# Kernel optimization log

Measured on AMD Instinct MI355X. Metric: run time of the kernel, lower is better.

The kernel has to match this reference:

```python
import jax, jax.numpy as jnp
import numpy as np

INV_DELTA = 15.0  # inv_delta init kwarg


def setup_inputs() -> dict:
    key = jax.random.key(0)
    k1, k2 = jax.random.split(key)
    features = jax.random.normal(k1, (64, 1024, 14, 14), dtype=jnp.float32)
    # torch init: randn(num_words, num_channels).clamp(min=0)
    embedding = jnp.clip(jax.random.normal(k2, (8192, 1024), dtype=jnp.float32), 0.0, None)
    min_distance_mean = jnp.ones((1,), dtype=jnp.float32) * 0.5  # buffer init
    return {"features": features, "embedding": embedding,
            "min_distance_mean": min_distance_mean}


def reference(features, embedding, min_distance_mean):
    # BoWExtractor.forward in eval mode (no dictionary queue update / EMA).
    f = features[:, :, 1:-1, 1:-1]                      # [B,C,12,12] crop border
    emb_sq = jnp.sum(embedding * embedding, axis=1)     # [K]  ||w_k||^2
    cross = jnp.einsum('bchw,kc->bkhw', f, embedding)   # 1x1 conv == GEMM
    # squared L2 distance to every codeword: [B,K,12,12]
    dist = jnp.sum(f * f, axis=1, keepdims=True) - 2.0 * cross \
           + emb_sq[None, :, None, None]
    inv_delta_adaptive = INV_DELTA / min_distance_mean[0]
    codes = jax.nn.softmax(-inv_delta_adaptive * dist, axis=1)  # soft assignment over K
    bow = jnp.max(codes, axis=(2, 3))                   # global max-pool -> [B,K]
    bow = bow / jnp.sum(jnp.abs(bow), axis=1, keepdims=True)  # L1 normalize
    return bow, codes
```

## Files before the change

### kernel.cpp

```cpp
#include <hip/hip_runtime.h>
#include <math.h>

#define BB   64
#define CC   1024
#define HWC  144
#define KK   8192
#define MM   9216
#define NBN  128

typedef __attribute__((ext_vector_type(8)))  short          bf16x8;
typedef __attribute__((ext_vector_type(8)))  unsigned short u16x8;
typedef __attribute__((ext_vector_type(4)))  unsigned short u16x4;
typedef __attribute__((ext_vector_type(4)))  float          f32x4;
typedef __attribute__((ext_vector_type(16))) float          f32x16;

#define FA_BYTES  ((size_t)MM * CC * 2 * 2)
#define FB_BYTES  ((size_t)KK * CC * 2 * 2)
#define OFF_FA    0
#define OFF_FB    (OFF_FA + FA_BYTES)
#define OFF_ESQ   (OFF_FB + FB_BYTES)
#define OFF_PM    (OFF_ESQ + (size_t)KK * 4)
#define OFF_PS    (OFF_PM + (size_t)NBN * MM * 4)
#define OFF_FACT  (OFF_PS + (size_t)NBN * MM * 4)
#define OFF_E     (OFF_FACT + (size_t)NBN * MM * 4)
#define E_BYTES   ((size_t)BB * KK * HWC * 2)
#define WS_NEED_B16 (OFF_E + E_BYTES)

__device__ inline unsigned short f2bf(float x) {
    union { float f; unsigned u; } v; v.f = x;
    unsigned r = v.u + 0x7fffu + ((v.u >> 16) & 1u);
    return (unsigned short)(r >> 16);
}
__device__ inline float bf2f(unsigned short h) {
    union { unsigned u; float f; } v; v.u = (unsigned)h << 16;
    return v.f;
}

__global__ __launch_bounds__(256)
void prep_A(const float* __restrict__ feat, u16x8* __restrict__ fA) {
    __shared__ float tile[64][145];
    int cb = blockIdx.x;
    int b  = blockIdx.y;
    for (int idx = threadIdx.x; idx < 64 * 144; idx += 256) {
        int r = idx / 144, hw = idx - r * 144;
        int h = hw / 12, w = hw - h * 12;
        tile[r][hw] = feat[(size_t)((b * 1024 + cb * 64 + r) * 196)
                           + (h + 1) * 14 + (w + 1)];
    }
    __syncthreads();
    for (int idx = threadIdx.x; idx < 8 * 144; idx += 256) {
        int g = idx / 144, hw = idx - g * 144;
        int p = b * 144 + hw;
        int bm = p >> 8, row = p & 255;
        int c = cb * 64 + g * 8;
        int kt = c >> 4, oct = (c >> 3) & 1;
        u16x8 hi, lo;
#pragma unroll
        for (int e = 0; e < 8; ++e) {
            float x = tile[g * 8 + e][hw];
            unsigned short h16 = f2bf(x);
            hi[e] = (short)h16;
            lo[e] = (short)f2bf(x - bf2f(h16));
        }
        size_t base = ((size_t)bm * 64 + kt) * 1024 + oct * 256 + row;
        fA[base] = hi;
        fA[base + 512] = lo;
    }
}

__global__ __launch_bounds__(256)
void prep_B(const float* __restrict__ emb, u16x8* __restrict__ fB) {
    __shared__ float tile[128][65];
    int cb = blockIdx.x;
    int nb = blockIdx.y;
#pragma unroll
    for (int i = 0; i < 8; ++i) {
        int idx = threadIdx.x + i * 256;
        int nl = idx >> 4, c4 = idx & 15;
        const float4 v = *reinterpret_cast<const float4*>(
            emb + (size_t)(nb * 128 + nl) * 1024 + cb * 64 + c4 * 4);
        tile[nl][c4 * 4 + 0] = v.x;
        tile[nl][c4 * 4 + 1] = v.y;
        tile[nl][c4 * 4 + 2] = v.z;
        tile[nl][c4 * 4 + 3] = v.w;
    }
    __syncthreads();
#pragma unroll
    for (int i = 0; i < 4; ++i) {
        int idx = threadIdx.x + i * 256;
        int kc = idx >> 7, rl = idx & 127;
        int c = cb * 64 + kc * 8;
        int kt = c >> 4, oct = (c >> 3) & 1;
        u16x8 hi, lo;
#pragma unroll
        for (int e = 0; e < 8; ++e) {
            float x = tile[rl][kc * 8 + e];
            unsigned short h16 = f2bf(x);
            hi[e] = (short)h16;
            lo[e] = (short)f2bf(x - bf2f(h16));
        }
        size_t base = ((size_t)nb * 64 + kt) * 512 + oct * 128 + rl;
        fB[base] = hi;
        fB[base + 256] = lo;
    }
}

__global__ void rowsumsq(const float* __restrict__ src, float* __restrict__ dst) {
    int row = blockIdx.x * 4 + (threadIdx.x >> 6);
    int l = threadIdx.x & 63;
    const float4* p = reinterpret_cast<const float4*>(src + (size_t)row * 1024);
    float s = 0.f;
#pragma unroll
    for (int it = 0; it < 4; ++it) {
        float4 v = p[l + it * 64];
        s += v.x * v.x + v.y * v.y + v.z * v.z + v.w * v.w;
    }
#pragma unroll
    for (int off = 32; off; off >>= 1) s += __shfl_down(s, off);
    if (l == 0) dst[row] = s;
}

__global__ __launch_bounds__(256, 2)
void gemm_mfma(const char* __restrict__ fA, const char* __restrict__ fB,
               const float* __restrict__ esq, const float* __restrict__ mdm,
               float* __restrict__ codes, float* __restrict__ pm,
               float* __restrict__ ps, unsigned short* __restrict__ Ebf,
               int ebf16) {
    __shared__ __align__(16) char smem[73728];

    int flat = blockIdx.x;
    int swz = (flat & 7) * 288 + (flat >> 3);
    int bm = swz >> 6, bn = swz & 63;

    int tid = threadIdx.x;
    int l = tid & 63, l31 = l & 31, lc2 = l >> 5;
    int wv = tid >> 6, wr = wv >> 1, wc = wv & 1;

    const char* gA = fA + (size_t)bm * 1048576;
    const char* gB = fB + (size_t)bn * 524288;

    f32x16 acc[4][2];
#pragma unroll
    for (int i = 0; i < 4; ++i)
#pragma unroll
        for (int j = 0; j < 2; ++j)
#pragma unroll
            for (int r = 0; r < 16; ++r) acc[i][j][r] = 0.f;

    auto stage = [&](int buf, int kt) {
        char* db = smem + buf * 24576;
        const char* ga = gA + (size_t)kt * 16384;
        const char* gb = gB + (size_t)kt * 8192;
#pragma unroll
        for (int i = 0; i < 4; ++i) {
            int off = i * 4096 + tid * 16;
            __builtin_amdgcn_global_load_lds(
                (const __attribute__((address_space(1))) void*)(ga + off),
                (__attribute__((address_space(3))) void*)(db + off), 16, 0, 0);
        }
#pragma unroll
        for (int i = 0; i < 2; ++i) {
            int off = i * 4096 + tid * 16;
            __builtin_amdgcn_global_load_lds(
                (const __attribute__((address_space(1))) void*)(gb + off),
                (__attribute__((address_space(3))) void*)(db + 16384 + off), 16, 0, 0);
        }
    };

    stage(0, 0);
    stage(1, 1);
    stage(2, 2);

    int cur = 0;
    for (int kt = 0; kt < 64; ++kt) {
        asm volatile("s_waitcnt vmcnt(12)" ::: "memory");
        __builtin_amdgcn_s_barrier();
        __builtin_amdgcn_sched_barrier(0);

        const char* bufc = smem + cur * 24576;
        bf16x8 ah[4], al[4], bh[2], bl[2];
#pragma unroll
        for (int f = 0; f < 4; ++f) {
            int ao = (lc2 * 256 + wr * 128 + f * 32 + l31) * 16;
            ah[f] = *(const bf16x8*)(bufc + ao);
            al[f] = *(const bf16x8*)(bufc + 8192 + ao);
        }
#pragma unroll
        for (int f = 0; f < 2; ++f) {
            int bo = 16384 + (lc2 * 128 + wc * 64 + f * 32 + l31) * 16;
            bh[f] = *(const bf16x8*)(bufc + bo);
            bl[f] = *(const bf16x8*)(bufc + 4096 + bo);
        }
        __builtin_amdgcn_s_setprio(1);
#pragma unroll
        for (int fi = 0; fi < 4; ++fi)
#pragma unroll
            for (int fj = 0; fj < 2; ++fj) {
                f32x16& A = acc[fi][fj];
                A = __builtin_amdgcn_mfma_f32_32x32x16_bf16(ah[fi], bh[fj], A, 0, 0, 0);
                A = __builtin_amdgcn_mfma_f32_32x32x16_bf16(ah[fi], bl[fj], A, 0, 0, 0);
                A = __builtin_amdgcn_mfma_f32_32x32x16_bf16(al[fi], bh[fj], A, 0, 0, 0);
            }
        __builtin_amdgcn_s_setprio(0);
        __builtin_amdgcn_s_barrier();
        int kn = (kt + 3 > 63) ? 63 : kt + 3;
        stage(cur, kn);
        cur = (cur == 2) ? 0 : cur + 1;
    }
    asm volatile("s_waitcnt vmcnt(0)" ::: "memory");

    float invl2 = (15.0f / mdm[0]) * 1.44269504089f;
    float s2 = 2.0f * invl2;
    float e2[2];
#pragma unroll
    for (int fj = 0; fj < 2; ++fj)
        e2[fj] = invl2 * esq[bn * 128 + wc * 64 + fj * 32 + l31];

    int bnp = bn * 2 + wc;

#pragma unroll
    for (int fi = 0; fi < 4; ++fi) {
        float mx[16], ss[16];
#pragma unroll
        for (int fj = 0; fj < 2; ++fj)
#pragma unroll
            for (int r = 0; r < 16; ++r)
                acc[fi][fj][r] = s2 * acc[fi][fj][r] - e2[fj];
#pragma unroll
        for (int r = 0; r < 16; ++r)
            mx[r] = fmaxf(acc[fi][0][r], acc[fi][1][r]);
#pragma unroll
        for (int off = 1; off < 32; off <<= 1)
#pragma unroll
            for (int r = 0; r < 16; ++r)
                mx[r] = fmaxf(mx[r], __shfl_xor(mx[r], off));
#pragma unroll
        for (int r = 0; r < 16; ++r) ss[r] = 0.f;
#pragma unroll
        for (int fj = 0; fj < 2; ++fj)
#pragma unroll
            for (int r = 0; r < 16; ++r) {
                float E = exp2f(acc[fi][fj][r] - mx[r]);
                acc[fi][fj][r] = E;
                ss[r] += E;
            }
#pragma unroll
        for (int off = 1; off < 32; off <<= 1)
#pragma unroll
            for (int r = 0; r < 16; ++r)
                ss[r] += __shfl_xor(ss[r], off);

        if (l31 == 0) {
#pragma unroll
            for (int r = 0; r < 16; ++r) {
                int row = wr * 128 + fi * 32 + 8 * (r >> 2) + 4 * lc2 + (r & 3);
                int p = bm * 256 + row;
                pm[(size_t)bnp * MM + p] = mx[r];
                ps[(size_t)bnp * MM + p] = ss[r];
            }
        }

        if (ebf16) {
#pragma unroll
            for (int fj = 0; fj < 2; ++fj) {
                int k = bn * 128 + wc * 64 + fj * 32 + l31;
#pragma unroll
                for (int q = 0; q < 4; ++q) {
                    int p0 = bm * 256 + wr * 128 + fi * 32 + 8 * q + 4 * lc2;
                    int b = p0 / 144, hw = p0 - b * 144;
                    u16x4 v;
                    v.x = f2bf(acc[fi][fj][q * 4 + 0]);
                    v.y = f2bf(acc[fi][fj][q * 4 + 1]);
                    v.z = f2bf(acc[fi][fj][q * 4 + 2]);
                    v.w = f2bf(acc[fi][fj][q * 4 + 3]);
                    __builtin_nontemporal_store(
                        v, (u16x4*)(Ebf + ((size_t)(b * 8192 + k)) * 144 + hw));
                }
            }
        } else {
#pragma unroll
            for (int fj = 0; fj < 2; ++fj) {
                int k = bn * 128 + wc * 64 + fj * 32 + l31;
#pragma unroll
                for (int q = 0; q < 4; ++q) {
                    int p0 = bm * 256 + wr * 128 + fi * 32 + 8 * q + 4 * lc2;
                    int b = p0 / 144, hw = p0 - b * 144;
                    f32x4 v;
                    v.x = acc[fi][fj][q * 4 + 0];
                    v.y = acc[fi][fj][q * 4 + 1];
                    v.z = acc[fi][fj][q * 4 + 2];
                    v.w = acc[fi][fj][q * 4 + 3];
                    __builtin_nontemporal_store(
                        v, (f32x4*)(codes + ((size_t)(b * 8192 + k)) * 144 + hw));
                }
            }
        }
    }
}

__global__ void comb_factor(const float* __restrict__ pm,
                            const float* __restrict__ ps,
                            float* __restrict__ factor) {
    int p = blockIdx.x * 256 + threadIdx.x;
    float m = -INFINITY;
#pragma unroll 8
    for (int bn = 0; bn < NBN; ++bn) m = fmaxf(m, pm[(size_t)bn * MM + p]);
    float S = 0.f;
#pragma unroll 8
    for (int bn = 0; bn < NBN; ++bn)
        S += ps[(size_t)bn * MM + p] * exp2f(pm[(size_t)bn * MM + p] - m);
    float is = 1.f / S;
#pragma unroll 8
    for (int bn = 0; bn < NBN; ++bn)
        factor[(size_t)bn * MM + p] = exp2f(pm[(size_t)bn * MM + p] - m) * is;
}

__global__ __launch_bounds__(256)
void scale_bow_b16(const unsigned short* __restrict__ E,
                   const float* __restrict__ factor,
                   float* __restrict__ codes, float* __restrict__ bow) {
    int wid = threadIdx.x >> 6, l = threadIdx.x & 63;
    int r = blockIdx.x * 4 + wid;
    int b = r >> 13, k = r & 8191;
    const u16x4* Ep = (const u16x4*)(E + (size_t)r * 144);
    f32x4* Cp = (f32x4*)(codes + (size_t)r * 144);
    const f32x4* Fp = (const f32x4*)(factor + (size_t)(k >> 6) * MM + b * 144);
    float m = 0.f;
    if (l < 36) {
        u16x4 e = __builtin_nontemporal_load(Ep + l);
        f32x4 f = Fp[l];
        f32x4 v;
        v.x = bf2f(e.x) * f.x;
        v.y = bf2f(e.y) * f.y;
        v.z = bf2f(e.z) * f.z;
        v.w = bf2f(e.w) * f.w;
        __builtin_nontemporal_store(v, Cp + l);
        m = fmaxf(fmaxf(v.x, v.y), fmaxf(v.z, v.w));
    }
#pragma unroll
    for (int off = 32; off; off >>= 1) m = fmaxf(m, __shfl_down(m, off));
    if (l == 0) bow[r] = m;
}

__global__ __launch_bounds__(256)
void scale_bow_f32(float* __restrict__ codes, const float* __restrict__ factor,
                   float* __restrict__ bow) {
    int wid = threadIdx.x >> 6, l = threadIdx.x & 63;
    int r = blockIdx.x * 4 + wid;
    int b = r >> 13, k = r & 8191;
    f32x4* Cp = (f32x4*)(codes + (size_t)r * 144);
    const f32x4* Fp = (const f32x4*)(factor + (size_t)(k >> 6) * MM + b * 144);
    float m = 0.f;
    if (l < 36) {
        f32x4 e = __builtin_nontemporal_load(Cp + l);
        f32x4 f = Fp[l];
        f32x4 v = e * f;
        __builtin_nontemporal_store(v, Cp + l);
        m = fmaxf(fmaxf(v.x, v.y), fmaxf(v.z, v.w));
    }
#pragma unroll
    for (int off = 32; off; off >>= 1) m = fmaxf(m, __shfl_down(m, off));
    if (l == 0) bow[r] = m;
}

__global__ void bow_norm(float* __restrict__ bow) {
    __shared__ float lds[4];
    __shared__ float stot;
    int b = blockIdx.x;
    float* p = bow + b * 8192;
    float s = 0.f;
    for (int i = threadIdx.x; i < 8192; i += 256) s += fabsf(p[i]);
#pragma unroll
    for (int off = 32; off; off >>= 1) s += __shfl_down(s, off);
    int wid = threadIdx.x >> 6, l = threadIdx.x & 63;
    if (l == 0) lds[wid] = s;
    __syncthreads();
    if (threadIdx.x == 0) stot = 1.f / (lds[0] + lds[1] + lds[2] + lds[3]);
    __syncthreads();
    float inv = stot;
    for (int i = threadIdx.x; i < 8192; i += 256) p[i] *= inv;
}

extern "C" void kernel_launch(void* const* d_in, const int* in_sizes, int n_in,
                              void* d_out, int out_size, void* d_ws, size_t ws_size,
                              hipStream_t stream) {
    const float* feat = (const float*)d_in[0];
    const float* emb  = (const float*)d_in[1];
    const float* mdm  = (const float*)d_in[2];
    float* bow   = (float*)d_out;
    float* codes = (float*)d_out + (size_t)BB * KK;

    char* ws = (char*)d_ws;
    u16x8* fA    = (u16x8*)(ws + OFF_FA);
    u16x8* fB    = (u16x8*)(ws + OFF_FB);
    float* esq   = (float*)(ws + OFF_ESQ);
    float* pm    = (float*)(ws + OFF_PM);
    float* ps    = (float*)(ws + OFF_PS);
    float* fact  = (float*)(ws + OFF_FACT);
    unsigned short* Ebf = (unsigned short*)(ws + OFF_E);

    int use_b16 = (ws_size >= WS_NEED_B16) ? 1 : 0;

    prep_A<<<dim3(16, 64), 256, 0, stream>>>(feat, fA);
    prep_B<<<dim3(16, 64), 256, 0, stream>>>(emb, fB);
    rowsumsq<<<KK / 4, 256, 0, stream>>>(emb, esq);
    gemm_mfma<<<2304, 256, 0, stream>>>((const char*)fA, (const char*)fB,
                                        esq, mdm, codes, pm, ps, Ebf, use_b16);
    comb_factor<<<36, 256, 0, stream>>>(pm, ps, fact);
    if (use_b16)
        scale_bow_b16<<<(BB * KK) / 4, 256, 0, stream>>>(Ebf, fact, codes, bow);
    else
        scale_bow_f32<<<(BB * KK) / 4, 256, 0, stream>>>(codes, fact, bow);
    bow_norm<<<BB, 256, 0, stream>>>(bow);
}
```

Before: 654.9 us.

## Enlarge GEMM tile to 256x256 with 8 waves and double-buffered 32-wide K stages

The GEMM block tile grows from 256x128 to 256x256 and runs with 512 threads (8 waves in a 2x4 grid). The packed embedding layout changes to match, and the K loop moves from a triple-buffered 16-wide stage to double-buffered 32-wide stages loaded in four chunks, interleaved with MFMA groups. The aim is more operand reuse per LDS load, less global traffic for the A operand, and better overlap of loads with MFMA work. The cost is 128KB of LDS per block, which likely allows only one block per CU despite the launch bound of 2, and a more fragile barrier and waitcnt schedule.

After: 737.6 us. 12.6% more time.

```diff
diff --git a/kernel.cpp b/kernel.cpp
--- a/kernel.cpp
+++ b/kernel.cpp
@@ -85,6 +85,7 @@
         tile[nl][c4 * 4 + 3] = v.w;
     }
     __syncthreads();
+    int bn = nb >> 1, colh = (nb & 1) * 128;
 #pragma unroll
     for (int i = 0; i < 4; ++i) {
         int idx = threadIdx.x + i * 256;
@@ -99,9 +100,9 @@
             hi[e] = (short)h16;
             lo[e] = (short)f2bf(x - bf2f(h16));
         }
-        size_t base = ((size_t)nb * 64 + kt) * 512 + oct * 128 + rl;
+        size_t base = ((size_t)bn * 64 + kt) * 1024 + oct * 256 + colh + rl;
         fB[base] = hi;
-        fB[base + 256] = lo;
+        fB[base + 512] = lo;
     }
 }
 
@@ -120,24 +121,24 @@
     if (l == 0) dst[row] = s;
 }
 
-__global__ __launch_bounds__(256, 2)
+__global__ __launch_bounds__(512, 2)
 void gemm_mfma(const char* __restrict__ fA, const char* __restrict__ fB,
                const float* __restrict__ esq, const float* __restrict__ mdm,
                float* __restrict__ codes, float* __restrict__ pm,
                float* __restrict__ ps, unsigned short* __restrict__ Ebf,
                int ebf16) {
-    __shared__ __align__(16) char smem[73728];
+    __shared__ __align__(16) char smem[131072];
 
     int flat = blockIdx.x;
-    int swz = (flat & 7) * 288 + (flat >> 3);
-    int bm = swz >> 6, bn = swz & 63;
+    int swz = (flat & 7) * 144 + (flat >> 3);
+    int bm = swz >> 5, bn = swz & 31;
 
     int tid = threadIdx.x;
-    int l = tid & 63, l31 = l & 31, lc2 = l >> 5;
-    int wv = tid >> 6, wr = wv >> 1, wc = wv & 1;
+    int l = tid & 63, l31 = l & 31, lc2 = (l >> 5) & 1;
+    int wv = tid >> 6, wr = wv >> 2, wc = wv & 3;
 
     const char* gA = fA + (size_t)bm * 1048576;
-    const char* gB = fB + (size_t)bn * 524288;
+    const char* gB = fB + (size_t)bn * 1048576;
 
     f32x16 acc[4][2];
 #pragma unroll
@@ -147,76 +148,88 @@
 #pragma unroll
             for (int r = 0; r < 16; ++r) acc[i][j][r] = 0.f;
 
-    auto stage = [&](int buf, int kt) {
-        char* db = smem + buf * 24576;
-        const char* ga = gA + (size_t)kt * 16384;
-        const char* gb = gB + (size_t)kt * 8192;
-#pragma unroll
-        for (int i = 0; i < 4; ++i) {
-            int off = i * 4096 + tid * 16;
+    auto chunkld = [&](int tn, int c) {
+        int ts = tn > 31 ? 31 : tn;
+        int kt2 = c >> 1;
+        const char* g = ((c & 1) ? gB : gA) + (size_t)ts * 32768 + kt2 * 16384;
+        char* d = smem + (tn & 1) * 65536 + ((c & 1) ? 32768 : 0) + kt2 * 16384;
+#pragma unroll
+        for (int r = 0; r < 2; ++r) {
+            int off = r * 8192 + tid * 16;
             __builtin_amdgcn_global_load_lds(
-                (const __attribute__((address_space(1))) void*)(ga + off),
-                (__attribute__((address_space(3))) void*)(db + off), 16, 0, 0);
-        }
-#pragma unroll
-        for (int i = 0; i < 2; ++i) {
-            int off = i * 4096 + tid * 16;
-            __builtin_amdgcn_global_load_lds(
-                (const __attribute__((address_space(1))) void*)(gb + off),
-                (__attribute__((address_space(3))) void*)(db + 16384 + off), 16, 0, 0);
+                (const __attribute__((address_space(1))) void*)(g + off),
+                (__attribute__((address_space(3))) void*)(d + off), 16, 0, 0);
         }
     };
 
-    stage(0, 0);
-    stage(1, 1);
-    stage(2, 2);
-
-    int cur = 0;
-    for (int kt = 0; kt < 64; ++kt) {
-        asm volatile("s_waitcnt vmcnt(12)" ::: "memory");
+    int aoff = lc2 * 4096 + (wr * 128 + l31) * 16;
+    int boff = lc2 * 4096 + (wc * 64 + l31) * 16;
+
+    chunkld(0, 0); chunkld(0, 1); chunkld(0, 2); chunkld(0, 3);
+    asm volatile("s_waitcnt vmcnt(4)" ::: "memory");
+    __builtin_amdgcn_s_barrier();
+
+#define READ_A(KT2, FI0)                                                     \
+    {                                                                        \
+        const char* p_ = bufc + (KT2) * 16384 + aoff + (FI0) * 512;          \
+        ah[0] = *(const bf16x8*)(p_);                                        \
+        al[0] = *(const bf16x8*)(p_ + 8192);                                 \
+        ah[1] = *(const bf16x8*)(p_ + 512);                                  \
+        al[1] = *(const bf16x8*)(p_ + 8192 + 512);                           \
+    }
+#define READ_B(KT2)                                                          \
+    {                                                                        \
+        const char* p_ = bufc + 32768 + (KT2) * 16384 + boff;                \
+        bh[0] = *(const bf16x8*)(p_);                                        \
+        bl[0] = *(const bf16x8*)(p_ + 8192);                                 \
+        bh[1] = *(const bf16x8*)(p_ + 512);                                  \
+        bl[1] = *(const bf16x8*)(p_ + 8192 + 512);                           \
+    }
+#define MFMA12(FI0)                                                          \
+    __builtin_amdgcn_s_setprio(1);                                           \
+    _Pragma("unroll")                                                        \
+    for (int i_ = 0; i_ < 2; ++i_) {                                         \
+        _Pragma("unroll")                                                    \
+        for (int fj_ = 0; fj_ < 2; ++fj_) {                                  \
+            f32x16& A_ = acc[(FI0) + i_][fj_];                               \
+            A_ = __builtin_amdgcn_mfma_f32_32x32x16_bf16(ah[i_], bh[fj_], A_, 0, 0, 0); \
+            A_ = __builtin_amdgcn_mfma_f32_32x32x16_bf16(ah[i_], bl[fj_], A_, 0, 0, 0); \
+            A_ = __builtin_amdgcn_mfma_f32_32x32x16_bf16(al[i_], bh[fj_], A_, 0, 0, 0); \
+        }                                                                    \
+    }                                                                        \
+    __builtin_amdgcn_s_setprio(0);
+
+    for (int t = 0; t < 32; ++t) {
+        const char* bufc = smem + (t & 1) * 65536;
+        bf16x8 ah[2], al[2], bh[2], bl[2];
+        READ_B(0); READ_A(0, 0);
+        chunkld(t + 1, 0);
         __builtin_amdgcn_s_barrier();
-        __builtin_amdgcn_sched_barrier(0);
-
-        const char* bufc = smem + cur * 24576;
-        bf16x8 ah[4], al[4], bh[2], bl[2];
-#pragma unroll
-        for (int f = 0; f < 4; ++f) {
-            int ao = (lc2 * 256 + wr * 128 + f * 32 + l31) * 16;
-            ah[f] = *(const bf16x8*)(bufc + ao);
-            al[f] = *(const bf16x8*)(bufc + 8192 + ao);
-        }
-#pragma unroll
-        for (int f = 0; f < 2; ++f) {
-            int bo = 16384 + (lc2 * 128 + wc * 64 + f * 32 + l31) * 16;
-            bh[f] = *(const bf16x8*)(bufc + bo);
-            bl[f] = *(const bf16x8*)(bufc + 4096 + bo);
-        }
-        __builtin_amdgcn_s_setprio(1);
-#pragma unroll
-        for (int fi = 0; fi < 4; ++fi)
-#pragma unroll
-            for (int fj = 0; fj < 2; ++fj) {
-                f32x16& A = acc[fi][fj];
-                A = __builtin_amdgcn_mfma_f32_32x32x16_bf16(ah[fi], bh[fj], A, 0, 0, 0);
-                A = __builtin_amdgcn_mfma_f32_32x32x16_bf16(ah[fi], bl[fj], A, 0, 0, 0);
-                A = __builtin_amdgcn_mfma_f32_32x32x16_bf16(al[fi], bh[fj], A, 0, 0, 0);
-            }
-        __builtin_amdgcn_s_setprio(0);
+        MFMA12(0)
+        READ_A(0, 2);
+        chunkld(t + 1, 1);
+        asm volatile("s_waitcnt vmcnt(4)" ::: "memory");
         __builtin_amdgcn_s_barrier();
-        int kn = (kt + 3 > 63) ? 63 : kt + 3;
-        stage(cur, kn);
-        cur = (cur == 2) ? 0 : cur + 1;
-    }
-    asm volatile("s_waitcnt vmcnt(0)" ::: "memory");
+        MFMA12(2)
+        READ_B(1); READ_A(1, 0);
+        chunkld(t + 1, 2);
+        __builtin_amdgcn_s_barrier();
+        MFMA12(0)
+        READ_A(1, 2);
+        chunkld(t + 1, 3);
+        asm volatile("s_waitcnt vmcnt(4)" ::: "memory");
+        __builtin_amdgcn_s_barrier();
+        MFMA12(2)
+    }
 
     float invl2 = (15.0f / mdm[0]) * 1.44269504089f;
     float s2 = 2.0f * invl2;
     float e2[2];
 #pragma unroll
     for (int fj = 0; fj < 2; ++fj)
-        e2[fj] = invl2 * esq[bn * 128 + wc * 64 + fj * 32 + l31];
-
-    int bnp = bn * 2 + wc;
+        e2[fj] = invl2 * esq[bn * 256 + wc * 64 + fj * 32 + l31];
+
+    int bnp = bn * 4 + wc;
 
 #pragma unroll
     for (int fi = 0; fi < 4; ++fi) {
@@ -263,7 +276,7 @@
         if (ebf16) {
 #pragma unroll
             for (int fj = 0; fj < 2; ++fj) {
-                int k = bn * 128 + wc * 64 + fj * 32 + l31;
+                int k = bn * 256 + wc * 64 + fj * 32 + l31;
 #pragma unroll
                 for (int q = 0; q < 4; ++q) {
                     int p0 = bm * 256 + wr * 128 + fi * 32 + 8 * q + 4 * lc2;
@@ -280,7 +293,7 @@
         } else {
 #pragma unroll
             for (int fj = 0; fj < 2; ++fj) {
-                int k = bn * 128 + wc * 64 + fj * 32 + l31;
+                int k = bn * 256 + wc * 64 + fj * 32 + l31;
 #pragma unroll
                 for (int q = 0; q < 4; ++q) {
                     int p0 = bm * 256 + wr * 128 + fi * 32 + 8 * q + 4 * lc2;
@@ -404,7 +417,7 @@
     prep_A<<<dim3(16, 64), 256, 0, stream>>>(feat, fA);
     prep_B<<<dim3(16, 64), 256, 0, stream>>>(emb, fB);
     rowsumsq<<<KK / 4, 256, 0, stream>>>(emb, esq);
-    gemm_mfma<<<2304, 256, 0, stream>>>((const char*)fA, (const char*)fB,
+    gemm_mfma<<<1152, 512, 0, stream>>>((const char*)fA, (const char*)fB,
                                         esq, mdm, codes, pm, ps, Ebf, use_b16);
     comb_factor<<<36, 256, 0, stream>>>(pm, ps, fact);
     if (use_b16)
```
